# Performance work log

Measured on AMD Instinct MI355X. Metric: run time of the kernel, lower is better.

## Reference

```python
import jax, jax.numpy as jnp
import numpy as np

B, S, D, H, DK, DFF = 4, 1024, 1024, 16, 64, 4096
EPS = 1e-5


def _layernorm(x, w, b):
    mu = jnp.mean(x, axis=-1, keepdims=True)
    var = jnp.mean((x - mu) ** 2, axis=-1, keepdims=True)
    return (x - mu) / jnp.sqrt(var + EPS) * w + b


def setup_inputs() -> dict:
    root = jax.random.key(0)
    ks = jax.random.split(root, 16)
    g = lambda k, shape, s=0.02: (jax.random.normal(k, shape, dtype=jnp.float32) * s)
    return {
        "mask": 1,
        "query": jax.random.normal(ks[0], (B, S, D), dtype=jnp.float32),
        "key": jax.random.normal(ks[1], (B, S, D), dtype=jnp.float32),
        "values": jax.random.normal(ks[2], (B, S, D), dtype=jnp.float32),
        "Wq": g(ks[3], (D, D)), "bq": jnp.zeros((D,), jnp.float32),
        "Wk": g(ks[4], (D, D)), "bk": jnp.zeros((D,), jnp.float32),
        "Wv": g(ks[5], (D, D)), "bv": jnp.zeros((D,), jnp.float32),
        "Wo": g(ks[6], (D, D)), "bo": jnp.zeros((D,), jnp.float32),
        "gammas": g(ks[7], (H, 1, 1), 0.5),
        "ln1_w": jnp.ones((D,), jnp.float32), "ln1_b": jnp.zeros((D,), jnp.float32),
        "W1": g(ks[8], (DFF, D)), "b1": jnp.zeros((DFF,), jnp.float32),
        "W2": g(ks[9], (D, DFF)), "b2": jnp.zeros((D,), jnp.float32),
        "ln2_w": jnp.ones((D,), jnp.float32), "ln2_b": jnp.zeros((D,), jnp.float32),
    }


def _forward(mask, query, key, values, Wq, bq, Wk, bk, Wv, bv, Wo, bo, gammas,
             ln1_w, ln1_b, W1, b1, W2, b2, ln2_w, ln2_b):
    # mask is a static Python int (the triu offset)
    allowed = jnp.triu(jnp.ones((S, S), dtype=jnp.float32), k=mask) == 0  # [S,S] bool

    def proj(x, W, b):  # [B,S,D] -> [B,H,S,DK]
        return (x @ W.T + b).reshape(B, S, H, DK).transpose(0, 2, 1, 3)

    q = proj(query, Wq, bq)
    k = proj(key, Wk, bk)
    v = proj(values, Wv, bv)

    scores = jnp.einsum('bhid,bhjd->bhij', q, k) / jnp.sqrt(jnp.float32(DK))

    # distance-decay factor, computed without gradient (torch.no_grad + detach)
    def dist_block(sc):
        sc_ = jax.nn.softmax(sc, axis=-1) * allowed.astype(sc.dtype)
        distcum = jnp.cumsum(sc_, axis=-1)
        disttot = jnp.sum(sc_, axis=-1, keepdims=True)
        idx = jnp.arange(S, dtype=jnp.float32)
        pos = jnp.abs(idx[None, :] - idx[:, None])[None, None]  # [1,1,S,S]
        return jnp.sqrt(jnp.clip((disttot - distcum) * pos, 0.0, None))
    dist_scores = jax.lax.stop_gradient(dist_block(scores))

    gamma = -jax.nn.softplus(gammas)[None]  # [1,H,1,1]
    total_effect = jnp.clip(jnp.exp(dist_scores * gamma), 1e-5, 1e5)
    scores = scores * total_effect
    scores = jnp.where(allowed, scores, jnp.float32(-1e20))
    attn = jax.nn.softmax(scores, axis=-1)
    if mask == 0:  # zero_pad first query row
        attn = attn.at[:, :, 0, :].set(0.0)

    out = jnp.einsum('bhij,bhjd->bhid', attn, v)
    concat = out.transpose(0, 2, 1, 3).reshape(B, S, D)
    attn_out = concat @ Wo.T + bo

    x = _layernorm(query + attn_out, ln1_w, ln1_b)
    ffn = jax.nn.relu(x @ W1.T + b1) @ W2.T + b2
    return _layernorm(x + ffn, ln2_w, ln2_b)


def reference(mask, query, key, values, Wq, bq, Wk, bk, Wv, bv, Wo, bo, gammas,
              ln1_w, ln1_b, W1, b1, W2, b2, ln2_w, ln2_b):
    return _forward(mask, query, key, values, Wq, bq, Wk, bk, Wv, bv, Wo, bo,
                    gammas, ln1_w, ln1_b, W1, b1, W2, b2, ln2_w, ln2_b)
```

## Files before the change

kernel.cpp:

```cpp
#include <hip/hip_runtime.h>
#include <hip/hip_bf16.h>
#include <math.h>

#define BB   4
#define SS   1024
#define DDIM 1024
#define HH   16
#define DKK  64
#define DFFF 4096
#define JC2  64

typedef __attribute__((ext_vector_type(8))) short short8;
typedef __attribute__((ext_vector_type(4))) float f32x4;
typedef unsigned short ushort;

__device__ __forceinline__ ushort f2bf(float f) {
    unsigned int u = __float_as_uint(f);
    unsigned int r = (u + 0x7FFFu + ((u >> 16) & 1u)) >> 16;
    return (ushort)r;
}
__device__ __forceinline__ short8 pack8(float4 f0, float4 f1) {
    short8 s;
    s[0] = (short)f2bf(f0.x); s[1] = (short)f2bf(f0.y);
    s[2] = (short)f2bf(f0.z); s[3] = (short)f2bf(f0.w);
    s[4] = (short)f2bf(f1.x); s[5] = (short)f2bf(f1.y);
    s[6] = (short)f2bf(f1.z); s[7] = (short)f2bf(f1.w);
    return s;
}

#define GLD16(g, l) __builtin_amdgcn_global_load_lds( \
    (const __attribute__((address_space(1))) unsigned int*)(g), \
    (__attribute__((address_space(3))) unsigned int*)(l), 16, 0, 0)

__device__ __forceinline__ float fexp2(float x) { return __builtin_amdgcn_exp2f(x); }

__device__ __forceinline__ float scan16(float x) {
    x += __int_as_float(__builtin_amdgcn_update_dpp(0, __float_as_int(x), 0x111, 0xF, 0xF, true));
    x += __int_as_float(__builtin_amdgcn_update_dpp(0, __float_as_int(x), 0x112, 0xF, 0xF, true));
    x += __int_as_float(__builtin_amdgcn_update_dpp(0, __float_as_int(x), 0x114, 0xF, 0xF, true));
    x += __int_as_float(__builtin_amdgcn_update_dpp(0, __float_as_int(x), 0x118, 0xF, 0xF, true));
    return x;
}
__device__ __forceinline__ float bcast15(float x) {
    return __int_as_float(__builtin_amdgcn_ds_swizzle(__float_as_int(x), 0x1F0));
}

__device__ __forceinline__ float block_reduce_sum(float v, float* red, int tid) {
#pragma unroll
    for (int off = 32; off; off >>= 1) v += __shfl_xor(v, off);
    __syncthreads();
    if ((tid & 63) == 0) red[tid >> 6] = v;
    __syncthreads();
    return red[0] + red[1] + red[2] + red[3];
}

struct CvtArgs { const float* s[9]; ushort* d[9]; unsigned int n[9]; };
__global__ __launch_bounds__(256) void convert_bf(CvtArgs a) {
    const int seg = blockIdx.y;
    size_t idx = ((size_t)blockIdx.x * 256 + threadIdx.x) * 8;
    if (idx >= a.n[seg]) return;
    const float* s = a.s[seg];
    float4 f0 = *(const float4*)(s + idx);
    float4 f1 = *(const float4*)(s + idx + 4);
    *(short8*)(a.d[seg] + idx) = pack8(f0, f1);
}

template <int BM, typename TC, bool RELU, bool BIAS>
__device__ __forceinline__ void gemm_core(const ushort* __restrict__ A, int lda,
                                          const ushort* __restrict__ Bm, int ldb,
                                          const float* __restrict__ bias,
                                          TC* __restrict__ C, int N, int Klen,
                                          int bm, int bn) {
    constexpr int MT = BM / 32;
    constexpr int PA = BM / 32;
    __shared__ ushort A_s[BM * 64];
    __shared__ ushort B_s[128 * 64];
    const int t = threadIdx.x;
    const int lane = t & 63, w = t >> 6;
    const int wr = w >> 1, wc = w & 1;
    const int fm = lane & 15, fq = lane >> 4;
    const int srl = lane >> 3;
    const int sg8 = ((lane & 7) ^ srl) << 3;

    f32x4 acc[MT][4];
#pragma unroll
    for (int mt = 0; mt < MT; mt++)
#pragma unroll
        for (int nt = 0; nt < 4; nt++) acc[mt][nt] = (f32x4){0.f, 0.f, 0.f, 0.f};

    for (int kt = 0; kt < Klen; kt += 64) {
        __syncthreads();
#pragma unroll
        for (int p = 0; p < PA; ++p) {
            int rowg = (w * PA + p) * 8;
            GLD16(A + (size_t)(bm + rowg + srl) * lda + kt + sg8, &A_s[rowg * 64]);
        }
#pragma unroll
        for (int p = 0; p < 4; ++p) {
            int rowg = (w * 4 + p) * 8;
            GLD16(Bm + (size_t)(bn + rowg + srl) * ldb + kt + sg8, &B_s[rowg * 64]);
        }
        __syncthreads();

        short8 av[2][MT], bv[2][4];
        const int sw = fm & 7;
#pragma unroll
        for (int mt = 0; mt < MT; ++mt) {
            int row = wr * (BM / 2) + mt * 16 + fm;
#pragma unroll
            for (int ks = 0; ks < 2; ++ks)
                av[ks][mt] = *(const short8*)&A_s[row * 64 + (((ks * 4 + fq) ^ sw) << 3)];
        }
#pragma unroll
        for (int nt = 0; nt < 4; ++nt) {
            int row = wc * 64 + nt * 16 + fm;
#pragma unroll
            for (int ks = 0; ks < 2; ++ks)
                bv[ks][nt] = *(const short8*)&B_s[row * 64 + (((ks * 4 + fq) ^ sw) << 3)];
        }
#pragma unroll
        for (int ks = 0; ks < 2; ++ks)
#pragma unroll
            for (int mt = 0; mt < MT; ++mt)
#pragma unroll
                for (int nt = 0; nt < 4; ++nt)
                    acc[mt][nt] = __builtin_amdgcn_mfma_f32_16x16x32_bf16(
                        av[ks][mt], bv[ks][nt], acc[mt][nt], 0, 0, 0);
    }

#pragma unroll
    for (int mt = 0; mt < MT; mt++) {
        int row0 = bm + wr * (BM / 2) + mt * 16 + fq * 4;
#pragma unroll
        for (int nt = 0; nt < 4; nt++) {
            int col = bn + wc * 64 + nt * 16 + fm;
            float bsv = BIAS ? bias[col] : 0.f;
#pragma unroll
            for (int r = 0; r < 4; r++) {
                float val = acc[mt][nt][r] + bsv;
                if (RELU) val = fmaxf(val, 0.f);
                if constexpr (sizeof(TC) == 4)
                    ((float*)C)[(size_t)(row0 + r) * N + col] = val;
                else
                    ((ushort*)C)[(size_t)(row0 + r) * N + col] = f2bf(val);
            }
        }
    }
}

template <int BM, typename TC, bool RELU>
__global__ __launch_bounds__(256, 2) void gemm_bf(const ushort* __restrict__ A,
                                                  const ushort* __restrict__ Bm,
                                                  const float* __restrict__ bias,
                                                  TC* __restrict__ C,
                                                  int N, int K) {
    gemm_core<BM, TC, RELU, true>(A, K, Bm, K, bias, C, N, K,
                                  blockIdx.y * BM, blockIdx.x * 128);
}

struct QkvArgs { const ushort* A[3]; const ushort* B[3]; const float* bias[3]; ushort* C[3]; };
__global__ __launch_bounds__(256, 2) void gemm_qkv(QkvArgs qa) {
    const int g = blockIdx.z;
    gemm_core<128, ushort, false, true>(qa.A[g], DDIM, qa.B[g], DDIM,
                                        qa.bias[g], qa.C[g], DDIM, DDIM,
                                        blockIdx.y * 128, blockIdx.x * 128);
}

struct SkArgs { const ushort* A; const ushort* Bm; float* C0; float* C1; int lda; int Klen; };
__global__ __launch_bounds__(256, 2) void gemm_splitk(SkArgs s) {
    const int z = blockIdx.z;
    float* C = z ? s.C1 : s.C0;
    const int koff = z * s.Klen;
    gemm_core<128, float, false, false>(s.A + koff, s.lda, s.Bm + koff, s.lda,
                                        nullptr, C, DDIM, s.Klen,
                                        blockIdx.y * 128, blockIdx.x * 128);
}

__global__ __launch_bounds__(256, 4) void attn_flash(
    const ushort* __restrict__ Q, const ushort* __restrict__ Kg,
    const ushort* __restrict__ Vg, const float* __restrict__ gammas,
    const int* __restrict__ maskp, ushort* __restrict__ out) {
    __shared__ short QP[64 * 72];
    __shared__ short Ks[JC2 * 72];
    __shared__ short Vts[64 * 72];

    const int t = threadIdx.x;
    const int lane = t & 63, w = t >> 6;
    const int col = lane & 15;
    const int quad = lane >> 4;

    const int bid = blockIdx.x;
    const int it = bid >> 6;
    const int bh = bid & 63;
    const int h = bh & (HH - 1);
    const int b = bh >> 4;
    const int i0 = it * 64;
    const int mask = *maskp;

    const float LOG2E = 1.44269504f;
    const float SC2 = 0.125f * LOG2E;
    const float g0 = gammas[h];
    const float gnat = -((g0 > 20.f) ? g0 : log1pf(__expf(g0)));
    const float g2 = gnat * LOG2E;

    const size_t qbase = ((size_t)(b * SS + i0)) * DDIM + h * DKK;
    const size_t kvbase = ((size_t)b * SS) * DDIM + h * DKK;

    {
        int r = t >> 2, d0 = (t & 3) << 4;
        const ushort* gq = Q + qbase + (size_t)r * DDIM + d0;
        *(short8*)&QP[r * 72 + d0]     = *(const short8*)(gq);
        *(short8*)&QP[r * 72 + d0 + 8] = *(const short8*)(gq + 8);
    }
    __syncthreads();
    const short8 qa0 = *(const short8*)&QP[(w * 16 + col) * 72 + quad * 8];
    const short8 qa1 = *(const short8*)&QP[(w * 16 + col) * 72 + 32 + quad * 8];

    float m1[4], su[4], smT[4], gi4[4];
    int lim4[4];
#pragma unroll
    for (int r = 0; r < 4; ++r) {
        m1[r] = -3.4e38f; su[r] = 0.f; smT[r] = 0.f;
        int gi = i0 + w * 16 + quad * 4 + r;
        gi4[r] = (float)gi;
        lim4[r] = gi + mask;
    }

    for (int ck = 0; ck < SS / JC2; ++ck) {
        const int jc = ck * JC2;
        __syncthreads();
        {
            int j = t >> 2, d0 = (t & 3) << 4;
            const ushort* gk = Kg + kvbase + (size_t)(jc + j) * DDIM + d0;
            *(short8*)&Ks[j * 72 + d0]     = *(const short8*)(gk);
            *(short8*)&Ks[j * 72 + d0 + 8] = *(const short8*)(gk + 8);
        }
        __syncthreads();
#pragma unroll
        for (int g = 0; g < 4; ++g) {
            short8 kb0 = *(const short8*)&Ks[(g * 16 + col) * 72 + quad * 8];
            short8 kb1 = *(const short8*)&Ks[(g * 16 + col) * 72 + 32 + quad * 8];
            f32x4 c = (f32x4){0.f, 0.f, 0.f, 0.f};
            c = __builtin_amdgcn_mfma_f32_16x16x32_bf16(qa0, kb0, c, 0, 0, 0);
            c = __builtin_amdgcn_mfma_f32_16x16x32_bf16(qa1, kb1, c, 0, 0, 0);
            int j = jc + g * 16 + col;
#pragma unroll
            for (int r = 0; r < 4; ++r) {
                float s2 = c[r] * SC2;
                m1[r] = fmaxf(m1[r], s2);
                float ev = fexp2(s2);
                su[r] += ev;
                smT[r] += (j < lim4[r]) ? ev : 0.f;
            }
        }
    }
#pragma unroll
    for (int off = 1; off < 16; off <<= 1) {
#pragma unroll
        for (int r = 0; r < 4; ++r) {
            m1[r] = fmaxf(m1[r], __shfl_xor(m1[r], off, 16));
            su[r] += __shfl_xor(su[r], off, 16);
            smT[r] += __shfl_xor(smT[r], off, 16);
        }
    }
    float lse2[4], smTn[4], ms2[4];
#pragma unroll
    for (int r = 0; r < 4; ++r) {
        lse2[r] = __log2f(su[r]);
        smTn[r] = smT[r] / su[r];
        ms2[r]  = fmaxf(m1[r], 0.f);
    }

    const int nck2 = min(SS / JC2, max(1, (i0 + 62 + mask) / 64 + 1));

    float l2[4], carry[4];
    f32x4 o[4];
#pragma unroll
    for (int r = 0; r < 4; ++r) { l2[r] = 0.f; carry[r] = 0.f; }
#pragma unroll
    for (int dg = 0; dg < 4; ++dg) o[dg] = (f32x4){0.f, 0.f, 0.f, 0.f};

    short* Pw = &QP[w * 16 * 72];

    for (int ck = 0; ck < nck2; ++ck) {
        const int jc = ck * JC2;
        __syncthreads();
        {
            int j = t >> 2, d0 = (t & 3) << 4;
            const ushort* gk = Kg + kvbase + (size_t)(jc + j) * DDIM + d0;
            *(short8*)&Ks[j * 72 + d0]     = *(const short8*)(gk);
            *(short8*)&Ks[j * 72 + d0 + 8] = *(const short8*)(gk + 8);
        }
        {
            int j = t & 63, dq = t >> 6, d0 = dq * 16;
            const ushort* gv = Vg + kvbase + (size_t)(jc + j) * DDIM + d0;
            short8 v0 = *(const short8*)(gv);
            short8 v1 = *(const short8*)(gv + 8);
#pragma unroll
            for (int k = 0; k < 8; ++k) {
                Vts[(d0 + k) * 72 + j]     = v0[k];
                Vts[(d0 + 8 + k) * 72 + j] = v1[k];
            }
        }
        __syncthreads();

#pragma unroll
        for (int g = 0; g < 4; ++g) {
            short8 kb0 = *(const short8*)&Ks[(g * 16 + col) * 72 + quad * 8];
            short8 kb1 = *(const short8*)&Ks[(g * 16 + col) * 72 + 32 + quad * 8];
            f32x4 c = (f32x4){0.f, 0.f, 0.f, 0.f};
            c = __builtin_amdgcn_mfma_f32_16x16x32_bf16(qa0, kb0, c, 0, 0, 0);
            c = __builtin_amdgcn_mfma_f32_16x16x32_bf16(qa1, kb1, c, 0, 0, 0);
            const int j = jc + g * 16 + col;
            const float jf = (float)j;
#pragma unroll
            for (int r = 0; r < 4; ++r) {
                float s2 = c[r] * SC2;
                float pj = fexp2(s2 - lse2[r]);
                float incl = (j < lim4[r]) ? pj : 0.f;
                incl = scan16(incl);
                float tot = bcast15(incl);
                float Cc = carry[r] + incl;
                carry[r] += tot;
                float pos = fabsf(jf - gi4[r]);
                float d2 = fmaxf((smTn[r] - Cc) * pos, 0.f);
                float dist = __builtin_amdgcn_sqrtf(d2);
                float eff = fmaxf(fexp2(g2 * dist), 1e-5f);
                float pe = fexp2(s2 * eff - ms2[r]);
                float p = (j < lim4[r]) ? pe : 0.f;
                l2[r] += p;
                Pw[(quad * 4 + r) * 72 + g * 16 + col] = (short)f2bf(p);
            }
        }
        __syncthreads();
#pragma unroll
        for (int kg = 0; kg < 2; ++kg) {
            short8 pa = *(const short8*)&Pw[col * 72 + kg * 32 + quad * 8];
#pragma unroll
            for (int dg = 0; dg < 4; ++dg) {
                short8 vb = *(const short8*)&Vts[(dg * 16 + col) * 72 + kg * 32 + quad * 8];
                o[dg] = __builtin_amdgcn_mfma_f32_16x16x32_bf16(pa, vb, o[dg], 0, 0, 0);
            }
        }
    }

#pragma unroll
    for (int off = 1; off < 16; off <<= 1)
#pragma unroll
        for (int r = 0; r < 4; ++r) l2[r] += __shfl_xor(l2[r], off, 16);

#pragma unroll
    for (int r = 0; r < 4; ++r) {
        int irow = i0 + w * 16 + quad * 4 + r;
        float scl = 1.f / l2[r];
        if (mask == 0 && irow == 0) scl = 0.f;
        size_t base = ((size_t)(b * SS) + irow) * DDIM + h * DKK;
#pragma unroll
        for (int dg = 0; dg < 4; ++dg)
            out[base + dg * 16 + col] = f2bf(o[dg][r] * scl);
    }
}

template <bool WB>
__global__ __launch_bounds__(256) void add_ln(const float* __restrict__ R,
                                              const float* __restrict__ Y0,
                                              const float* __restrict__ Y1,
                                              const float* __restrict__ gb,
                                              const float* __restrict__ w,
                                              const float* __restrict__ bb,
                                              float* __restrict__ out,
                                              ushort* __restrict__ obf) {
    const int row = blockIdx.x;
    const int tid = threadIdx.x;
    __shared__ float red[4];
    __shared__ float xs[DDIM];
    const size_t base = (size_t)row * DDIM;
    float s = 0.f, s2 = 0.f;
#pragma unroll
    for (int l = 0; l < 4; l++) {
        int idx = tid + l * 256;
        float x = R[base + idx] + Y0[base + idx] + Y1[base + idx] + gb[idx];
        xs[idx] = x;
        s += x;
        s2 += x * x;
    }
    s = block_reduce_sum(s, red, tid);
    s2 = block_reduce_sum(s2, red, tid);
    const float mu = s * (1.f / DDIM);
    const float var = s2 * (1.f / DDIM) - mu * mu;
    const float rstd = rsqrtf(var + 1e-5f);
#pragma unroll
    for (int l = 0; l < 4; l++) {
        int idx = tid + l * 256;
        float v = (xs[idx] - mu) * rstd * w[idx] + bb[idx];
        out[base + idx] = v;
        if (WB) obf[base + idx] = f2bf(v);
    }
}

extern "C" void kernel_launch(void* const* d_in, const int* in_sizes, int n_in,
                              void* d_out, int out_size, void* d_ws, size_t ws_size,
                              hipStream_t stream) {
    const int*   maskp  = (const int*)d_in[0];
    const float* query  = (const float*)d_in[1];
    const float* key    = (const float*)d_in[2];
    const float* values = (const float*)d_in[3];
    const float* Wq = (const float*)d_in[4];
    const float* bq = (const float*)d_in[5];
    const float* Wk = (const float*)d_in[6];
    const float* bk = (const float*)d_in[7];
    const float* Wv = (const float*)d_in[8];
    const float* bv = (const float*)d_in[9];
    const float* Wo = (const float*)d_in[10];
    const float* bo = (const float*)d_in[11];
    const float* gammas = (const float*)d_in[12];
    const float* ln1w = (const float*)d_in[13];
    const float* ln1b = (const float*)d_in[14];
    const float* W1 = (const float*)d_in[15];
    const float* b1 = (const float*)d_in[16];
    const float* W2 = (const float*)d_in[17];
    const float* b2 = (const float*)d_in[18];
    const float* ln2w = (const float*)d_in[19];
    const float* ln2b = (const float*)d_in[20];

    const int M = BB * SS;
    const size_t MB = 1048576;
    char* wsb = (char*)d_ws;
    ushort* Wq_bf = (ushort*)(wsb + 0 * MB);
    ushort* Wk_bf = (ushort*)(wsb + 8 * MB);
    ushort* Wv_bf = (ushort*)(wsb + 16 * MB);
    ushort* Wo_bf = (ushort*)(wsb + 24 * MB);
    ushort* W1_bf = (ushort*)(wsb + 32 * MB);
    ushort* W2_bf = (ushort*)(wsb + 40 * MB);
    ushort* qi_bf = (ushort*)(wsb + 48 * MB);
    ushort* ki_bf = (ushort*)(wsb + 56 * MB);
    ushort* vi_bf = (ushort*)(wsb + 64 * MB);
    ushort* Qb    = (ushort*)(wsb + 72 * MB);
    ushort* Kb    = (ushort*)(wsb + 80 * MB);
    ushort* Vb    = (ushort*)(wsb + 88 * MB);
    ushort* ATTb  = (ushort*)(wsb + 96 * MB);
    float*  Ysp0  = (float*)(wsb + 104 * MB);
    float*  Ysp1  = (float*)(wsb + 0 * MB);
    float*  xf    = (float*)(wsb + 48 * MB);
    ushort* x_bf  = (ushort*)(wsb + 64 * MB);
    ushort* hidden= (ushort*)(wsb + 72 * MB);

    dim3 blk(256);

    const unsigned int N4M = 4u * 1024 * 1024, N1M = 1024 * 1024;
    CvtArgs ca;
    ca.s[0] = query; ca.s[1] = key; ca.s[2] = values;
    ca.s[3] = Wq; ca.s[4] = Wk; ca.s[5] = Wv; ca.s[6] = Wo;
    ca.s[7] = W1; ca.s[8] = W2;
    ca.d[0] = qi_bf; ca.d[1] = ki_bf; ca.d[2] = vi_bf;
    ca.d[3] = Wq_bf; ca.d[4] = Wk_bf; ca.d[5] = Wv_bf; ca.d[6] = Wo_bf;
    ca.d[7] = W1_bf; ca.d[8] = W2_bf;
    ca.n[0] = N4M; ca.n[1] = N4M; ca.n[2] = N4M;
    ca.n[3] = N1M; ca.n[4] = N1M; ca.n[5] = N1M; ca.n[6] = N1M;
    ca.n[7] = N4M; ca.n[8] = N4M;
    convert_bf<<<dim3(2048, 9), blk, 0, stream>>>(ca);

    QkvArgs qa;
    qa.A[0] = qi_bf; qa.A[1] = ki_bf; qa.A[2] = vi_bf;
    qa.B[0] = Wq_bf; qa.B[1] = Wk_bf; qa.B[2] = Wv_bf;
    qa.bias[0] = bq; qa.bias[1] = bk; qa.bias[2] = bv;
    qa.C[0] = Qb; qa.C[1] = Kb; qa.C[2] = Vb;
    gemm_qkv<<<dim3(8, 32, 3), blk, 0, stream>>>(qa);

    attn_flash<<<dim3(BB * HH * 16), blk, 0, stream>>>(Qb, Kb, Vb, gammas, maskp, ATTb);

    {
        SkArgs s; s.A = ATTb; s.Bm = Wo_bf; s.C0 = Ysp0; s.C1 = Ysp1;
        s.lda = DDIM; s.Klen = DDIM / 2;
        gemm_splitk<<<dim3(8, 32, 2), blk, 0, stream>>>(s);
    }

    add_ln<true><<<dim3(M), blk, 0, stream>>>(query, Ysp0, Ysp1, bo, ln1w, ln1b, xf, x_bf);

    gemm_bf<128, ushort, true><<<dim3(32, 32), blk, 0, stream>>>(x_bf, W1_bf, b1, hidden, DFFF, DDIM);

    {
        SkArgs s; s.A = hidden; s.Bm = W2_bf; s.C0 = Ysp0; s.C1 = Ysp1;
        s.lda = DFFF; s.Klen = DFFF / 2;
        gemm_splitk<<<dim3(8, 32, 2), blk, 0, stream>>>(s);
    }

    add_ln<false><<<dim3(M), blk, 0, stream>>>(xf, Ysp0, Ysp1, b2, ln2w, ln2b, (float*)d_out, nullptr);
}
```

Measured before the change: 411.1 us.

## Fuse fp32-to-bf16 activation conversion into QKV GEMM loads and reorder attention tiles

The QKV projection GEMM now reads query/key/values in fp32 directly, converting to bf16 in registers before writing to shared memory. This removes the separate conversion pass over the three activation tensors (write and re-read of 24 MB). The cost is that the A-tile loads become synchronous register loads instead of direct global-to-LDS loads, and each A tile is converted once per N-block. The attention kernel's block-to-tile mapping is also permuted so causal tiles of different lengths are interleaved, which should balance work across CUs.

```diff
diff --git a/kernel.cpp b/kernel.cpp
--- a/kernel.cpp
+++ b/kernel.cpp
@@ -54,7 +54,7 @@
     return red[0] + red[1] + red[2] + red[3];
 }
 
-struct CvtArgs { const float* s[9]; ushort* d[9]; unsigned int n[9]; };
+struct CvtArgs { const float* s[6]; ushort* d[6]; unsigned int n[6]; };
 __global__ __launch_bounds__(256) void convert_bf(CvtArgs a) {
     const int seg = blockIdx.y;
     size_t idx = ((size_t)blockIdx.x * 256 + threadIdx.x) * 8;
@@ -65,8 +65,8 @@
     *(short8*)(a.d[seg] + idx) = pack8(f0, f1);
 }
 
-template <int BM, typename TC, bool RELU, bool BIAS>
-__device__ __forceinline__ void gemm_core(const ushort* __restrict__ A, int lda,
+template <int BM, typename TC, bool RELU, bool BIAS, bool CVTA>
+__device__ __forceinline__ void gemm_core(const void* __restrict__ Av, int lda,
                                           const ushort* __restrict__ Bm, int ldb,
                                           const float* __restrict__ bias,
                                           TC* __restrict__ C, int N, int Klen,
@@ -90,10 +90,23 @@
 
     for (int kt = 0; kt < Klen; kt += 64) {
         __syncthreads();
-#pragma unroll
-        for (int p = 0; p < PA; ++p) {
-            int rowg = (w * PA + p) * 8;
-            GLD16(A + (size_t)(bm + rowg + srl) * lda + kt + sg8, &A_s[rowg * 64]);
+        if constexpr (CVTA) {
+            const float* Af = (const float*)Av;
+#pragma unroll
+            for (int p = 0; p < PA; ++p) {
+                int rowg = (w * PA + p) * 8;
+                const float* src = Af + (size_t)(bm + rowg + srl) * lda + kt + sg8;
+                float4 f0 = *(const float4*)(src);
+                float4 f1 = *(const float4*)(src + 4);
+                *(short8*)&A_s[(rowg + srl) * 64 + ((lane & 7) << 3)] = pack8(f0, f1);
+            }
+        } else {
+            const ushort* A = (const ushort*)Av;
+#pragma unroll
+            for (int p = 0; p < PA; ++p) {
+                int rowg = (w * PA + p) * 8;
+                GLD16(A + (size_t)(bm + rowg + srl) * lda + kt + sg8, &A_s[rowg * 64]);
+            }
         }
 #pragma unroll
         for (int p = 0; p < 4; ++p) {
@@ -154,16 +167,16 @@
                                                   const float* __restrict__ bias,
                                                   TC* __restrict__ C,
                                                   int N, int K) {
-    gemm_core<BM, TC, RELU, true>(A, K, Bm, K, bias, C, N, K,
-                                  blockIdx.y * BM, blockIdx.x * 128);
-}
-
-struct QkvArgs { const ushort* A[3]; const ushort* B[3]; const float* bias[3]; ushort* C[3]; };
+    gemm_core<BM, TC, RELU, true, false>(A, K, Bm, K, bias, C, N, K,
+                                         blockIdx.y * BM, blockIdx.x * 128);
+}
+
+struct QkvArgs { const float* A[3]; const ushort* B[3]; const float* bias[3]; ushort* C[3]; };
 __global__ __launch_bounds__(256, 2) void gemm_qkv(QkvArgs qa) {
     const int g = blockIdx.z;
-    gemm_core<128, ushort, false, true>(qa.A[g], DDIM, qa.B[g], DDIM,
-                                        qa.bias[g], qa.C[g], DDIM, DDIM,
-                                        blockIdx.y * 128, blockIdx.x * 128);
+    gemm_core<128, ushort, false, true, true>(qa.A[g], DDIM, qa.B[g], DDIM,
+                                              qa.bias[g], qa.C[g], DDIM, DDIM,
+                                              blockIdx.y * 128, blockIdx.x * 128);
 }
 
 struct SkArgs { const ushort* A; const ushort* Bm; float* C0; float* C1; int lda; int Klen; };
@@ -171,9 +184,9 @@
     const int z = blockIdx.z;
     float* C = z ? s.C1 : s.C0;
     const int koff = z * s.Klen;
-    gemm_core<128, float, false, false>(s.A + koff, s.lda, s.Bm + koff, s.lda,
-                                        nullptr, C, DDIM, s.Klen,
-                                        blockIdx.y * 128, blockIdx.x * 128);
+    gemm_core<128, float, false, false, false>(s.A + koff, s.lda, s.Bm + koff, s.lda,
+                                               nullptr, C, DDIM, s.Klen,
+                                               blockIdx.y * 128, blockIdx.x * 128);
 }
 
 __global__ __launch_bounds__(256, 4) void attn_flash(
@@ -190,8 +203,10 @@
     const int quad = lane >> 4;
 
     const int bid = blockIdx.x;
-    const int it = bid >> 6;
-    const int bh = bid & 63;
+    const int q4 = bid >> 8;
+    const int rr = bid & 255;
+    const int it = q4 * 4 + ((rr + q4) & 3);
+    const int bh = rr >> 2;
     const int h = bh & (HH - 1);
     const int b = bh >> 4;
     const int i0 = it * 64;
@@ -432,15 +447,12 @@
     ushort* Wo_bf = (ushort*)(wsb + 24 * MB);
     ushort* W1_bf = (ushort*)(wsb + 32 * MB);
     ushort* W2_bf = (ushort*)(wsb + 40 * MB);
-    ushort* qi_bf = (ushort*)(wsb + 48 * MB);
-    ushort* ki_bf = (ushort*)(wsb + 56 * MB);
-    ushort* vi_bf = (ushort*)(wsb + 64 * MB);
     ushort* Qb    = (ushort*)(wsb + 72 * MB);
     ushort* Kb    = (ushort*)(wsb + 80 * MB);
     ushort* Vb    = (ushort*)(wsb + 88 * MB);
     ushort* ATTb  = (ushort*)(wsb + 96 * MB);
     float*  Ysp0  = (float*)(wsb + 104 * MB);
-    float*  Ysp1  = (float*)(wsb + 0 * MB);
+    float*  Ysp1  = (float*)(wsb + 120 * MB);
     float*  xf    = (float*)(wsb + 48 * MB);
     ushort* x_bf  = (ushort*)(wsb + 64 * MB);
     ushort* hidden= (ushort*)(wsb + 72 * MB);
@@ -449,19 +461,16 @@
 
     const unsigned int N4M = 4u * 1024 * 1024, N1M = 1024 * 1024;
     CvtArgs ca;
-    ca.s[0] = query; ca.s[1] = key; ca.s[2] = values;
-    ca.s[3] = Wq; ca.s[4] = Wk; ca.s[5] = Wv; ca.s[6] = Wo;
-    ca.s[7] = W1; ca.s[8] = W2;
-    ca.d[0] = qi_bf; ca.d[1] = ki_bf; ca.d[2] = vi_bf;
-    ca.d[3] = Wq_bf; ca.d[4] = Wk_bf; ca.d[5] = Wv_bf; ca.d[6] = Wo_bf;
-    ca.d[7] = W1_bf; ca.d[8] = W2_bf;
-    ca.n[0] = N4M; ca.n[1] = N4M; ca.n[2] = N4M;
-    ca.n[3] = N1M; ca.n[4] = N1M; ca.n[5] = N1M; ca.n[6] = N1M;
-    ca.n[7] = N4M; ca.n[8] = N4M;
-    convert_bf<<<dim3(2048, 9), blk, 0, stream>>>(ca);
+    ca.s[0] = Wq; ca.s[1] = Wk; ca.s[2] = Wv; ca.s[3] = Wo;
+    ca.s[4] = W1; ca.s[5] = W2;
+    ca.d[0] = Wq_bf; ca.d[1] = Wk_bf; ca.d[2] = Wv_bf; ca.d[3] = Wo_bf;
+    ca.d[4] = W1_bf; ca.d[5] = W2_bf;
+    ca.n[0] = N1M; ca.n[1] = N1M; ca.n[2] = N1M; ca.n[3] = N1M;
+    ca.n[4] = N4M; ca.n[5] = N4M;
+    convert_bf<<<dim3(2048, 6), blk, 0, stream>>>(ca);
 
     QkvArgs qa;
-    qa.A[0] = qi_bf; qa.A[1] = ki_bf; qa.A[2] = vi_bf;
+    qa.A[0] = query; qa.A[1] = key; qa.A[2] = values;
     qa.B[0] = Wq_bf; qa.B[1] = Wk_bf; qa.B[2] = Wv_bf;
     qa.bias[0] = bq; qa.bias[1] = bk; qa.bias[2] = bv;
     qa.C[0] = Qb; qa.C[1] = Kb; qa.C[2] = Vb;
```

Measured after the change: 410.4 us. About the same (-0.2%).
